# Optimization experiments

Measured on AMD Instinct MI355X. Metric: run time of the kernel, lower is better.

The kernel has to match this reference:

```python
import jax, jax.numpy as jnp
import numpy as np

N_NODES, N_EDGES = 100000, 800000
F_NODE, F_EDGE, N_CLASSES = 128, 16, 10


def _lin(key, fan_in, fan_out, bias=True):
    k1, k2 = jax.random.split(key)
    W = jax.random.normal(k1, (fan_in, fan_out), jnp.float32) * 0.05
    if bias:
        b = jax.random.normal(k2, (fan_out,), jnp.float32) * 0.05
        return W, b
    return (W,)


def setup_inputs() -> dict:
    key = jax.random.key(0)
    ks = jax.random.split(key, 24)
    inp = {
        "x": jax.random.normal(ks[0], (N_NODES, F_NODE), jnp.float32),
        "edge_index": jax.random.randint(ks[1], (2, N_EDGES), 0, N_NODES, jnp.int64 if jax.config.jax_enable_x64 else jnp.int32),
        "edge_attr": jax.random.normal(ks[2], (N_EDGES, F_EDGE), jnp.float32),
    }
    dims = [(F_NODE, 128), (128, 128), (128, 256)]  # (in_channels, out_channels) per layer
    i = 3
    for li, (din, dout) in enumerate(dims, start=1):
        inp[f"Wq{li}"], inp[f"bq{li}"] = _lin(ks[i], din, dout); i += 1
        inp[f"Wk{li}"], inp[f"bk{li}"] = _lin(ks[i], din, dout); i += 1
        inp[f"Wv{li}"], inp[f"bv{li}"] = _lin(ks[i], din, dout); i += 1
        (inp[f"We{li}"],) = _lin(ks[i], F_EDGE, dout, bias=False); i += 1  # PyG lin_edge: bias=False
        inp[f"Ws{li}"], inp[f"bs{li}"] = _lin(ks[i], din, dout); i += 1  # root/skip weight
    inp["Wc"], inp["bc"] = _lin(ks[i], 256, N_CLASSES)
    return inp


def transformer_conv(x, src, dst, edge_attr, Wq, bq, Wk, bk, Wv, bv, We, Ws, bs):
    """PyG TransformerConv, heads=1, concat=True, root_weight=True."""
    N = x.shape[0]
    C = Wq.shape[1]
    q = x @ Wq + bq                      # [N, C]
    k = x @ Wk + bk                      # [N, C]
    v = x @ Wv + bv                      # [N, C]
    e = edge_attr @ We                   # [E, C] edge-conditioned term
    # per-edge attention logits: <q_i, k_j + e_ij> / sqrt(C)
    alpha = jnp.sum(q[dst] * (k[src] + e), axis=-1) / jnp.sqrt(jnp.float32(C))  # [E]
    # segment softmax over edges sharing a destination node
    m = jax.ops.segment_max(alpha, dst, num_segments=N)
    p = jnp.exp(alpha - m[dst])
    s = jax.ops.segment_sum(p, dst, num_segments=N)
    a = p / (s[dst] + 1e-16)
    # scatter-aggregate weighted messages (value_j + edge term)
    out = jax.ops.segment_sum(a[:, None] * (v[src] + e), dst, num_segments=N)  # [N, C]
    return out + x @ Ws + bs             # root/skip connection


def reference(x, edge_index, edge_attr,
              Wq1, bq1, Wk1, bk1, Wv1, bv1, We1, Ws1, bs1,
              Wq2, bq2, Wk2, bk2, Wv2, bv2, We2, Ws2, bs2,
              Wq3, bq3, Wk3, bk3, Wv3, bv3, We3, Ws3, bs3,
              Wc, bc):
    src, dst = edge_index[0], edge_index[1]
    h = transformer_conv(x, src, dst, edge_attr, Wq1, bq1, Wk1, bk1, Wv1, bv1, We1, Ws1, bs1)
    h = jax.nn.relu(h)  # dropout is identity in eval mode
    h = transformer_conv(h, src, dst, edge_attr, Wq2, bq2, Wk2, bk2, Wv2, bv2, We2, Ws2, bs2)
    h = jax.nn.relu(h)
    h = transformer_conv(h, src, dst, edge_attr, Wq3, bq3, Wk3, bk3, Wv3, bv3, We3, Ws3, bs3)
    return h @ Wc + bc                   # [N, num_classes]
```

## Files before the change

kernel.cpp:

```cpp
#include <hip/hip_runtime.h>
#include <math.h>


typedef unsigned int uint;
typedef unsigned short ushort;
typedef __bf16 bf16x8 __attribute__((ext_vector_type(8)));
typedef float f32x4 __attribute__((ext_vector_type(4)));

__device__ __forceinline__ ushort f2bf(float f) {
    uint u = __float_as_uint(f);
    u += 0x7fffu + ((u >> 16) & 1u);
    return (ushort)(u >> 16);
}
__device__ __forceinline__ float bf2f(ushort h) {
    return __uint_as_float(((uint)h) << 16);
}
__device__ __forceinline__ void unpack8(uint4 t, float* o) {
    o[0] = bf2f((ushort)(t.x & 0xffffu)); o[1] = bf2f((ushort)(t.x >> 16));
    o[2] = bf2f((ushort)(t.y & 0xffffu)); o[3] = bf2f((ushort)(t.y >> 16));
    o[4] = bf2f((ushort)(t.z & 0xffffu)); o[5] = bf2f((ushort)(t.z >> 16));
    o[6] = bf2f((ushort)(t.w & 0xffffu)); o[7] = bf2f((ushort)(t.w >> 16));
}

__global__ void k_zero(uint* p, int n) {
    int i = blockIdx.x * 256 + threadIdx.x;
    if (i < n) p[i] = 0u;
}

__global__ void k_hist(const int* __restrict__ dst, uint* __restrict__ counts, int E, int N) {
    int e = blockIdx.x * 256 + threadIdx.x;
    if (e < E) {
        int d = dst[e];
        d = (d < 0) ? 0 : (d >= N ? N - 1 : d);
        atomicAdd(&counts[d], 1u);
    }
}

__global__ void k_scan1(const uint* __restrict__ counts, uint* __restrict__ bsum, int n) {
    __shared__ uint sm[256];
    int tid = threadIdx.x;
    int base = blockIdx.x * 1024 + tid * 4;
    uint s = 0;
#pragma unroll
    for (int j = 0; j < 4; ++j)
        if (base + j < n) s += counts[base + j];
    sm[tid] = s;
    __syncthreads();
    for (int d = 128; d > 0; d >>= 1) {
        if (tid < d) sm[tid] += sm[tid + d];
        __syncthreads();
    }
    if (tid == 0) bsum[blockIdx.x] = sm[0];
}

__global__ void k_scan2(uint* bsum, int nb) {
    if (threadIdx.x == 0 && blockIdx.x == 0) {
        uint run = 0;
        for (int i = 0; i < nb; ++i) { uint v = bsum[i]; bsum[i] = run; run += v; }
    }
}

__global__ void k_scan3(const uint* __restrict__ counts, const uint* __restrict__ bsum,
                        uint* __restrict__ row_ptr, int n, int E) {
    __shared__ uint sm[256];
    int tid = threadIdx.x;
    int base = blockIdx.x * 1024 + tid * 4;
    uint local[4];
    uint s = 0;
#pragma unroll
    for (int j = 0; j < 4; ++j) {
        local[j] = (base + j < n) ? counts[base + j] : 0u;
        s += local[j];
    }
    sm[tid] = s;
    __syncthreads();
    for (int d = 1; d < 256; d <<= 1) {
        uint v = (tid >= d) ? sm[tid - d] : 0u;
        __syncthreads();
        sm[tid] += v;
        __syncthreads();
    }
    uint run = sm[tid] - s + bsum[blockIdx.x];
#pragma unroll
    for (int j = 0; j < 4; ++j)
        if (base + j < n) { row_ptr[base + j] = run; run += local[j]; }
    if (blockIdx.x == 0 && tid == 0) row_ptr[n] = (uint)E;
}

__global__ void k_fill(const int* __restrict__ ei, const uint* __restrict__ row_ptr,
                       uint* __restrict__ cursor, int2* __restrict__ srcid, int E, int N) {
    int e = blockIdx.x * 256 + threadIdx.x;
    if (e >= E) return;
    int s = ei[e];
    int d = ei[E + e];
    s = (s < 0) ? 0 : (s >= N ? N - 1 : s);
    d = (d < 0) ? 0 : (d >= N ? N - 1 : d);
    uint idx = row_ptr[d] + atomicAdd(&cursor[d], 1u);
    srcid[idx] = make_int2(s, e);
}

__global__ void k_cvt(const float4* __restrict__ in, ushort4* __restrict__ outp, int n4) {
    int i = blockIdx.x * 256 + threadIdx.x;
    if (i >= n4) return;
    float4 v = in[i];
    ushort4 o;
    o.x = f2bf(v.x); o.y = f2bf(v.y); o.z = f2bf(v.z); o.w = f2bf(v.w);
    outp[i] = o;
}

__global__ void k_packg(const float* __restrict__ Wq, const float* __restrict__ bq,
                        const float* __restrict__ We, float* __restrict__ Wgf,
                        float* __restrict__ bgf, int C) {
    int id = blockIdx.x * 256 + threadIdx.x;
    if (id < 2048) {
        int k = id >> 4, f = id & 15;
        float s = 0.f;
        for (int c = 0; c < C; ++c) s = fmaf(Wq[k * C + c], We[f * C + c], s);
        Wgf[id] = s;
    } else if (id < 2064) {
        int f = id - 2048;
        float s = 0.f;
        for (int c = 0; c < C; ++c) s = fmaf(bq[c], We[f * C + c], s);
        bgf[f] = s;
    }
}

__global__ void k_packw(const float* __restrict__ Wq, const float* __restrict__ Wk,
                        const float* __restrict__ Wv, const float* __restrict__ Ws,
                        const float* __restrict__ Wgf, ushort* __restrict__ Bp, int C) {
    int nct = (4 * C + 16) >> 4;
    int total = 4 * nct * 512;
    int id = blockIdx.x * 256 + threadIdx.x;
    if (id >= total) return;
    int j = id & 7;
    int rest = id >> 3;
    int lane = rest & 63;
    rest >>= 6;
    int ct = rest % nct;
    int kt = rest / nct;
    int k = kt * 32 + ((lane >> 4) << 3) + j;
    int c = (ct << 4) + (lane & 15);
    float w;
    if (c < 4 * C) {
        int mat = c / C, cc = c % C;
        const float* W = (mat == 0) ? Wq : (mat == 1) ? Wk : (mat == 2) ? Wv : Ws;
        w = W[k * C + cc];
    } else {
        w = Wgf[k * 16 + (c - 4 * C)];
    }
    Bp[id] = f2bf(w);
}

__global__ void k_bias(const float* __restrict__ bq, const float* __restrict__ bk,
                       const float* __restrict__ bv, const float* __restrict__ bs,
                       const float* __restrict__ bgf, float* __restrict__ outp, int C) {
    int c = blockIdx.x * 256 + threadIdx.x;
    if (c >= 4 * C + 16) return;
    float v;
    if (c < 4 * C) {
        int mat = c / C, cc = c % C;
        const float* b = (mat == 0) ? bq : (mat == 1) ? bk : (mat == 2) ? bv : bs;
        v = b[cc];
    } else {
        v = bgf[c - 4 * C];
    }
    outp[c] = v;
}

__global__ __launch_bounds__(256) void k_gemm(const ushort* __restrict__ A,
                                              const ushort* __restrict__ Bp,
                                              const float* __restrict__ bias,
                                              ushort* __restrict__ H,
                                              ushort* __restrict__ S,
                                              ushort* __restrict__ g, int C) {
    int fourC = 4 * C, threeC = 3 * C;
    int P = fourC + 16;
    int nct = P >> 4;
    int lane = threadIdx.x & 63;
    int wave = threadIdx.x >> 6;
    int quad = lane >> 4;
    int r = lane & 15;
    int m0 = blockIdx.y << 4;
    int c0 = (blockIdx.x << 8) + (wave << 6);
    int ct0 = c0 >> 4;
    if (ct0 >= nct) return;
    int row = m0 + r;

    f32x4 acc[4];
#pragma unroll
    for (int i = 0; i < 4; ++i) acc[i] = (f32x4){0.f, 0.f, 0.f, 0.f};

#pragma unroll
    for (int kk = 0; kk < 4; ++kk) {
        bf16x8 a = *(const bf16x8*)(A + (size_t)row * 128 + kk * 32 + (quad << 3));
#pragma unroll
        for (int i = 0; i < 4; ++i) {
            if (ct0 + i < nct) {
                bf16x8 b = *(const bf16x8*)(Bp + ((size_t)((kk * nct + ct0 + i) << 6) + lane) * 8);
                acc[i] = __builtin_amdgcn_mfma_f32_16x16x32_bf16(a, b, acc[i], 0, 0, 0);
            }
        }
    }
#pragma unroll
    for (int i = 0; i < 4; ++i) {
        int cc = c0 + (i << 4) + r;
        if (cc >= P) continue;
        float bi = bias[cc];
#pragma unroll
        for (int reg = 0; reg < 4; ++reg) {
            int rr = m0 + (quad << 2) + reg;
            ushort val = f2bf(acc[i][reg] + bi);
            if (cc < threeC)      H[(size_t)rr * threeC + cc] = val;
            else if (cc < fourC)  S[(size_t)rr * C + (cc - threeC)] = val;
            else                  g[(size_t)rr * 16 + (cc - fourC)] = val;
        }
    }
}

template <int C, int GSIZE, bool RELU>
__global__ __launch_bounds__(256, 6) void k_edge(const ushort* __restrict__ H,
                                                 ushort* __restrict__ S,
                                                 const ushort* __restrict__ g,
                                                 const uint* __restrict__ row_ptr,
                                                 const int2* __restrict__ srcid,
                                                 const float* __restrict__ eattr,
                                                 const float* __restrict__ We,
                                                 int N) {
    constexpr int VR = C / GSIZE;
    constexpr int TH = 3 * C;
    constexpr int GPB = 256 / GSIZE;
    __shared__ float swex[GPB][17];
    const float scale = (C == 128) ? 0.08838834764831843f : 0.0625f;
    const float foldk = 16.0f / (float)GSIZE;

    int lane = threadIdx.x & (GSIZE - 1);
    int grp = threadIdx.x / GSIZE;
    int f = lane & 15;
    int node = blockIdx.x * GPB + grp;
    if (node >= N) return;

    float q[VR];
    {
        uint4 tt = *(const uint4*)(H + (size_t)node * TH + lane * VR);
        unpack8(tt, q);
    }
    float gl = bf2f(g[(size_t)node * 16 + f]);
    uint beg = row_ptr[node], end = row_ptr[node + 1];

    float l = 0.f, w = 0.f;
    float acc[VR];
#pragma unroll
    for (int j = 0; j < VR; ++j) acc[j] = 0.f;

    for (uint t = beg; t < end; t += 2) {
        bool has1 = (t + 1 < end);
        int2 se0 = srcid[t];
        int2 se1 = has1 ? srcid[t + 1] : se0;
        float at0 = eattr[(size_t)se0.y * 16 + f];
        float at1 = eattr[(size_t)se1.y * 16 + f];
        uint4 k0 = *(const uint4*)(H + (size_t)se0.x * TH + C + lane * VR);
        uint4 v0 = *(const uint4*)(H + (size_t)se0.x * TH + 2 * C + lane * VR);
        uint4 k1, v1;
        if (has1) {
            k1 = *(const uint4*)(H + (size_t)se1.x * TH + C + lane * VR);
            v1 = *(const uint4*)(H + (size_t)se1.x * TH + 2 * C + lane * VR);
        }
        float kf[VR];
        unpack8(k0, kf);
        float p0 = foldk * at0 * gl;
#pragma unroll
        for (int j = 0; j < VR; ++j) p0 = fmaf(q[j], kf[j], p0);
        float p1 = 0.f;
        if (has1) {
            unpack8(k1, kf);
            p1 = foldk * at1 * gl;
#pragma unroll
            for (int j = 0; j < VR; ++j) p1 = fmaf(q[j], kf[j], p1);
        }
        p0 += __shfl_xor(p0, 1); p1 += __shfl_xor(p1, 1);
        p0 += __shfl_xor(p0, 2); p1 += __shfl_xor(p1, 2);
        p0 += __shfl_xor(p0, 4); p1 += __shfl_xor(p1, 4);
        p0 += __shfl_xor(p0, 8); p1 += __shfl_xor(p1, 8);
        if (GSIZE == 32) { p0 += __shfl_xor(p0, 16); p1 += __shfl_xor(p1, 16); }
        float e0 = __expf(p0 * scale);
        float e1 = has1 ? __expf(p1 * scale) : 0.f;
        l += e0 + e1;
        w = fmaf(e0, at0, w);
        w = fmaf(e1, at1, w);
        float vf[VR];
        unpack8(v0, vf);
#pragma unroll
        for (int j = 0; j < VR; ++j) acc[j] = fmaf(e0, vf[j], acc[j]);
        if (has1) {
            unpack8(v1, vf);
#pragma unroll
            for (int j = 0; j < VR; ++j) acc[j] = fmaf(e1, vf[j], acc[j]);
        }
    }

    float inv = 1.f / (l + 1e-16f);
    if (lane < 16) swex[grp][lane] = w;
    float ew[VR];
#pragma unroll
    for (int j = 0; j < VR; ++j) ew[j] = 0.f;
#pragma unroll
    for (int f2 = 0; f2 < 16; ++f2) {
        float wf = swex[grp][f2];
        const float* wrow = We + f2 * C + lane * VR;
#pragma unroll
        for (int u = 0; u < VR / 4; ++u) {
            float4 cv = *(const float4*)(wrow + u * 4);
            ew[u * 4 + 0] = fmaf(wf, cv.x, ew[u * 4 + 0]);
            ew[u * 4 + 1] = fmaf(wf, cv.y, ew[u * 4 + 1]);
            ew[u * 4 + 2] = fmaf(wf, cv.z, ew[u * 4 + 2]);
            ew[u * 4 + 3] = fmaf(wf, cv.w, ew[u * 4 + 3]);
        }
    }
    ushort* srow = S + (size_t)node * C + lane * VR;
    uint4 skv = *(const uint4*)srow;
    float sk[8];
    unpack8(skv, sk);
    uint4 ov;
    uint* op = (uint*)&ov;
#pragma unroll
    for (int h = 0; h < 4; ++h) {
        float o0 = (acc[2 * h] + ew[2 * h]) * inv + sk[2 * h];
        float o1 = (acc[2 * h + 1] + ew[2 * h + 1]) * inv + sk[2 * h + 1];
        if (RELU) { o0 = fmaxf(o0, 0.f); o1 = fmaxf(o1, 0.f); }
        op[h] = (uint)f2bf(o0) | ((uint)f2bf(o1) << 16);
    }
    *(uint4*)srow = ov;
}

__global__ void k_cls(const ushort* __restrict__ h, const float* __restrict__ Wc,
                      const float* __restrict__ bc, float* __restrict__ outp, int N) {
    int t = blockIdx.x * 256 + threadIdx.x;
    int node = t >> 4;
    int c = t & 15;
    if (node >= N || c >= 10) return;
    const ushort* hr = h + (size_t)node * 256;
    float acc = 0.f;
#pragma unroll 4
    for (int k4 = 0; k4 < 64; ++k4) {
        uint2 u = *(const uint2*)(hr + k4 * 4);
        float h0 = bf2f((ushort)(u.x & 0xffffu));
        float h1 = bf2f((ushort)(u.x >> 16));
        float h2 = bf2f((ushort)(u.y & 0xffffu));
        float h3 = bf2f((ushort)(u.y >> 16));
        int kb = k4 * 4;
        acc = fmaf(h0, Wc[(kb + 0) * 10 + c], acc);
        acc = fmaf(h1, Wc[(kb + 1) * 10 + c], acc);
        acc = fmaf(h2, Wc[(kb + 2) * 10 + c], acc);
        acc = fmaf(h3, Wc[(kb + 3) * 10 + c], acc);
    }
    outp[node * 10 + c] = acc + bc[c];
}

extern "C" void kernel_launch(void* const* d_in, const int* in_sizes, int n_in,
                              void* d_out, int out_size, void* d_ws, size_t ws_size,
                              hipStream_t stream) {
    const float* x = (const float*)d_in[0];
    const int* ei = (const int*)d_in[1];
    const float* eattr = (const float*)d_in[2];
    const int N = in_sizes[0] / 128;
    const int E = in_sizes[1] / 2;

    const float* Wq[3], *bq[3], *Wk[3], *bk[3], *Wv[3], *bv[3], *We[3], *Ws[3], *bs[3];
    for (int li = 0; li < 3; ++li) {
        int base = 3 + li * 9;
        Wq[li] = (const float*)d_in[base + 0];
        bq[li] = (const float*)d_in[base + 1];
        Wk[li] = (const float*)d_in[base + 2];
        bk[li] = (const float*)d_in[base + 3];
        Wv[li] = (const float*)d_in[base + 4];
        bv[li] = (const float*)d_in[base + 5];
        We[li] = (const float*)d_in[base + 6];
        Ws[li] = (const float*)d_in[base + 7];
        bs[li] = (const float*)d_in[base + 8];
    }
    const float* Wc = (const float*)d_in[30];
    const float* bc = (const float*)d_in[31];

    size_t off = 0;
    char* base = (char*)d_ws;
    auto alloc = [&](size_t bytes) -> void* {
        void* p = base + off;
        off = (off + bytes + 255) & ~(size_t)255;
        return p;
    };
    ushort* SA = (ushort*)alloc((size_t)N * 256 * 2);
    ushort* SB = (ushort*)alloc((size_t)N * 128 * 2);
    ushort* H  = (ushort*)alloc((size_t)N * 768 * 2);
    ushort* gbuf = (ushort*)alloc((size_t)N * 16 * 2);
    ushort* Bp = (ushort*)alloc(140000 * 2);
    float* biasc = (float*)alloc(1040 * 4);
    float* Wgf = (float*)alloc(2048 * 4);
    float* bgf = (float*)alloc(16 * 4);
    uint* row_ptr = (uint*)alloc((size_t)(N + 1) * 4);
    uint* counts = (uint*)alloc((size_t)N * 4);
    uint* cursor = (uint*)alloc((size_t)N * 4);
    uint* bsum = (uint*)alloc(1024 * 4);
    int2* srcid = (int2*)alloc((size_t)E * 8);

    ushort* xb = SB;

    int nb = (N + 1023) / 1024;

    k_zero<<<(N + 255) / 256, 256, 0, stream>>>(counts, N);
    k_zero<<<(N + 255) / 256, 256, 0, stream>>>(cursor, N);
    k_hist<<<(E + 255) / 256, 256, 0, stream>>>(ei + E, counts, E, N);
    k_scan1<<<nb, 256, 0, stream>>>(counts, bsum, N);
    k_scan2<<<1, 64, 0, stream>>>(bsum, nb);
    k_scan3<<<nb, 256, 0, stream>>>(counts, bsum, row_ptr, N, E);
    k_fill<<<(E + 255) / 256, 256, 0, stream>>>(ei, row_ptr, cursor, srcid, E, N);

    int n4 = N * 128 / 4;
    k_cvt<<<(n4 + 255) / 256, 256, 0, stream>>>((const float4*)x, (ushort4*)xb, n4);

    for (int li = 0; li < 3; ++li) {
        int C = (li == 2) ? 256 : 128;
        int P = 4 * C + 16;
        int packTotal = 4 * (P >> 4) * 512;
        const ushort* A = (li == 0) ? xb : (li == 1) ? SA : SB;
        ushort* Sout = (li == 1) ? SB : SA;

        k_packg<<<9, 256, 0, stream>>>(Wq[li], bq[li], We[li], Wgf, bgf, C);
        k_packw<<<(packTotal + 255) / 256, 256, 0, stream>>>(Wq[li], Wk[li], Wv[li], Ws[li], Wgf, Bp, C);
        k_bias<<<(P + 255) / 256, 256, 0, stream>>>(bq[li], bk[li], bv[li], bs[li], bgf, biasc, C);
        k_gemm<<<dim3((P + 255) / 256, N / 16), 256, 0, stream>>>(A, Bp, biasc, H, Sout, gbuf, C);
        if (li == 2)
            k_edge<256, 32, false><<<(N * 32 + 255) / 256, 256, 0, stream>>>(H, Sout, gbuf, row_ptr, srcid, eattr, We[li], N);
        else
            k_edge<128, 16, true><<<(N * 16 + 255) / 256, 256, 0, stream>>>(H, Sout, gbuf, row_ptr, srcid, eattr, We[li], N);
    }

    k_cls<<<(N * 16 + 255) / 256, 256, 0, stream>>>(SA, Wc, bc, (float*)d_out, N);
}
```

Baseline: 1.030 ms.

## Switch intermediates from bf16 to fp16 and unroll edge loop by four

Stores projected node features in fp16 instead of bf16, uses the fp16 MFMA for the fused projection GEMM, and computes attention dot products with packed fdot2 instructions. The edge aggregation loop now handles four edges per iteration with clamped indices, which raises memory-level parallelism for the gathered K/V rows. Value accumulation and the edge-term expansion use packed two-wide float FMAs. Activations that exceed the fp16 range could overflow, and the wider unroll raises register pressure.

```diff
diff --git a/kernel.cpp b/kernel.cpp
--- a/kernel.cpp
+++ b/kernel.cpp
@@ -4,23 +4,31 @@
 
 typedef unsigned int uint;
 typedef unsigned short ushort;
-typedef __bf16 bf16x8 __attribute__((ext_vector_type(8)));
+typedef _Float16 f16x8 __attribute__((ext_vector_type(8)));
+typedef _Float16 h16x2 __attribute__((ext_vector_type(2)));
 typedef float f32x4 __attribute__((ext_vector_type(4)));
-
-__device__ __forceinline__ ushort f2bf(float f) {
-    uint u = __float_as_uint(f);
-    u += 0x7fffu + ((u >> 16) & 1u);
-    return (ushort)(u >> 16);
-}
-__device__ __forceinline__ float bf2f(ushort h) {
-    return __uint_as_float(((uint)h) << 16);
-}
-__device__ __forceinline__ void unpack8(uint4 t, float* o) {
-    o[0] = bf2f((ushort)(t.x & 0xffffu)); o[1] = bf2f((ushort)(t.x >> 16));
-    o[2] = bf2f((ushort)(t.y & 0xffffu)); o[3] = bf2f((ushort)(t.y >> 16));
-    o[4] = bf2f((ushort)(t.z & 0xffffu)); o[5] = bf2f((ushort)(t.z >> 16));
-    o[6] = bf2f((ushort)(t.w & 0xffffu)); o[7] = bf2f((ushort)(t.w >> 16));
-}
+typedef float f32x2 __attribute__((ext_vector_type(2)));
+
+__device__ __forceinline__ ushort f2h(float f) {
+    return __builtin_bit_cast(ushort, (_Float16)f);
+}
+__device__ __forceinline__ float h2f(ushort h) {
+    return (float)__builtin_bit_cast(_Float16, h);
+}
+__device__ __forceinline__ h16x2 bch2(uint u) { return __builtin_bit_cast(h16x2, u); }
+__device__ __forceinline__ f32x2 cvt2(uint u) {
+    h16x2 h = bch2(u);
+    return (f32x2){(float)h.x, (float)h.y};
+}
+
+#if __has_builtin(__builtin_amdgcn_fdot2)
+#define FDOT2(a, b, c) __builtin_amdgcn_fdot2((a), (b), (c), false)
+#else
+__device__ __forceinline__ float fdot2_sw(h16x2 a, h16x2 b, float c) {
+    return fmaf((float)a.x, (float)b.x, fmaf((float)a.y, (float)b.y, c));
+}
+#define FDOT2(a, b, c) fdot2_sw((a), (b), (c))
+#endif
 
 __global__ void k_zero(uint* p, int n) {
     int i = blockIdx.x * 256 + threadIdx.x;
@@ -104,7 +112,7 @@
     if (i >= n4) return;
     float4 v = in[i];
     ushort4 o;
-    o.x = f2bf(v.x); o.y = f2bf(v.y); o.z = f2bf(v.z); o.w = f2bf(v.w);
+    o.x = f2h(v.x); o.y = f2h(v.y); o.z = f2h(v.z); o.w = f2h(v.w);
     outp[i] = o;
 }
 
@@ -148,7 +156,7 @@
     } else {
         w = Wgf[k * 16 + (c - 4 * C)];
     }
-    Bp[id] = f2bf(w);
+    Bp[id] = f2h(w);
 }
 
 __global__ void k_bias(const float* __restrict__ bq, const float* __restrict__ bk,
@@ -192,12 +200,12 @@
 
 #pragma unroll
     for (int kk = 0; kk < 4; ++kk) {
-        bf16x8 a = *(const bf16x8*)(A + (size_t)row * 128 + kk * 32 + (quad << 3));
+        f16x8 a = *(const f16x8*)(A + (size_t)row * 128 + kk * 32 + (quad << 3));
 #pragma unroll
         for (int i = 0; i < 4; ++i) {
             if (ct0 + i < nct) {
-                bf16x8 b = *(const bf16x8*)(Bp + ((size_t)((kk * nct + ct0 + i) << 6) + lane) * 8);
-                acc[i] = __builtin_amdgcn_mfma_f32_16x16x32_bf16(a, b, acc[i], 0, 0, 0);
+                f16x8 b = *(const f16x8*)(Bp + ((size_t)((kk * nct + ct0 + i) << 6) + lane) * 8);
+                acc[i] = __builtin_amdgcn_mfma_f32_16x16x32_f16(a, b, acc[i], 0, 0, 0);
             }
         }
     }
@@ -209,7 +217,7 @@
 #pragma unroll
         for (int reg = 0; reg < 4; ++reg) {
             int rr = m0 + (quad << 2) + reg;
-            ushort val = f2bf(acc[i][reg] + bi);
+            ushort val = f2h(acc[i][reg] + bi);
             if (cc < threeC)      H[(size_t)rr * threeC + cc] = val;
             else if (cc < fourC)  S[(size_t)rr * C + (cc - threeC)] = val;
             else                  g[(size_t)rr * 16 + (cc - fourC)] = val;
@@ -238,96 +246,117 @@
     int f = lane & 15;
     int node = blockIdx.x * GPB + grp;
     if (node >= N) return;
-
-    float q[VR];
-    {
-        uint4 tt = *(const uint4*)(H + (size_t)node * TH + lane * VR);
-        unpack8(tt, q);
-    }
-    float gl = bf2f(g[(size_t)node * 16 + f]);
+    int lvr = lane * VR;
+
+    uint4 qv = *(const uint4*)(H + (size_t)node * TH + lvr);
+    h16x2 q0 = bch2(qv.x), q1 = bch2(qv.y), q2 = bch2(qv.z), q3 = bch2(qv.w);
+    float gl = h2f(g[(size_t)node * 16 + f]);
+    float fg = foldk * gl;
     uint beg = row_ptr[node], end = row_ptr[node + 1];
 
     float l = 0.f, w = 0.f;
-    float acc[VR];
-#pragma unroll
-    for (int j = 0; j < VR; ++j) acc[j] = 0.f;
-
-    for (uint t = beg; t < end; t += 2) {
-        bool has1 = (t + 1 < end);
-        int2 se0 = srcid[t];
-        int2 se1 = has1 ? srcid[t + 1] : se0;
-        float at0 = eattr[(size_t)se0.y * 16 + f];
-        float at1 = eattr[(size_t)se1.y * 16 + f];
-        uint4 k0 = *(const uint4*)(H + (size_t)se0.x * TH + C + lane * VR);
-        uint4 v0 = *(const uint4*)(H + (size_t)se0.x * TH + 2 * C + lane * VR);
-        uint4 k1, v1;
-        if (has1) {
-            k1 = *(const uint4*)(H + (size_t)se1.x * TH + C + lane * VR);
-            v1 = *(const uint4*)(H + (size_t)se1.x * TH + 2 * C + lane * VR);
+    f32x2 acc[4];
+#pragma unroll
+    for (int j = 0; j < 4; ++j) acc[j] = (f32x2){0.f, 0.f};
+
+    for (uint t = beg; t < end; t += 4) {
+        uint t1 = (t + 1 < end) ? t + 1 : t;
+        uint t2 = (t + 2 < end) ? t + 2 : t;
+        uint t3 = (t + 3 < end) ? t + 3 : t;
+        int2 s0 = srcid[t], s1 = srcid[t1], s2 = srcid[t2], s3 = srcid[t3];
+        float at0 = eattr[(size_t)s0.y * 16 + f];
+        float at1 = eattr[(size_t)s1.y * 16 + f];
+        float at2 = eattr[(size_t)s2.y * 16 + f];
+        float at3 = eattr[(size_t)s3.y * 16 + f];
+        const ushort* hb0 = H + (size_t)s0.x * TH + C + lvr;
+        const ushort* hb1 = H + (size_t)s1.x * TH + C + lvr;
+        const ushort* hb2 = H + (size_t)s2.x * TH + C + lvr;
+        const ushort* hb3 = H + (size_t)s3.x * TH + C + lvr;
+        uint4 k0 = *(const uint4*)hb0, v0 = *(const uint4*)(hb0 + C);
+        uint4 k1 = *(const uint4*)hb1, v1 = *(const uint4*)(hb1 + C);
+        uint4 k2 = *(const uint4*)hb2, v2 = *(const uint4*)(hb2 + C);
+        uint4 k3 = *(const uint4*)hb3, v3 = *(const uint4*)(hb3 + C);
+
+        float p0 = at0 * fg, p1 = at1 * fg, p2 = at2 * fg, p3 = at3 * fg;
+        p0 = FDOT2(q0, bch2(k0.x), p0); p0 = FDOT2(q1, bch2(k0.y), p0);
+        p0 = FDOT2(q2, bch2(k0.z), p0); p0 = FDOT2(q3, bch2(k0.w), p0);
+        p1 = FDOT2(q0, bch2(k1.x), p1); p1 = FDOT2(q1, bch2(k1.y), p1);
+        p1 = FDOT2(q2, bch2(k1.z), p1); p1 = FDOT2(q3, bch2(k1.w), p1);
+        p2 = FDOT2(q0, bch2(k2.x), p2); p2 = FDOT2(q1, bch2(k2.y), p2);
+        p2 = FDOT2(q2, bch2(k2.z), p2); p2 = FDOT2(q3, bch2(k2.w), p2);
+        p3 = FDOT2(q0, bch2(k3.x), p3); p3 = FDOT2(q1, bch2(k3.y), p3);
+        p3 = FDOT2(q2, bch2(k3.z), p3); p3 = FDOT2(q3, bch2(k3.w), p3);
+
+        p0 += __shfl_xor(p0, 1); p1 += __shfl_xor(p1, 1);
+        p2 += __shfl_xor(p2, 1); p3 += __shfl_xor(p3, 1);
+        p0 += __shfl_xor(p0, 2); p1 += __shfl_xor(p1, 2);
+        p2 += __shfl_xor(p2, 2); p3 += __shfl_xor(p3, 2);
+        p0 += __shfl_xor(p0, 4); p1 += __shfl_xor(p1, 4);
+        p2 += __shfl_xor(p2, 4); p3 += __shfl_xor(p3, 4);
+        p0 += __shfl_xor(p0, 8); p1 += __shfl_xor(p1, 8);
+        p2 += __shfl_xor(p2, 8); p3 += __shfl_xor(p3, 8);
+        if (GSIZE == 32) {
+            p0 += __shfl_xor(p0, 16); p1 += __shfl_xor(p1, 16);
+            p2 += __shfl_xor(p2, 16); p3 += __shfl_xor(p3, 16);
         }
-        float kf[VR];
-        unpack8(k0, kf);
-        float p0 = foldk * at0 * gl;
-#pragma unroll
-        for (int j = 0; j < VR; ++j) p0 = fmaf(q[j], kf[j], p0);
-        float p1 = 0.f;
-        if (has1) {
-            unpack8(k1, kf);
-            p1 = foldk * at1 * gl;
-#pragma unroll
-            for (int j = 0; j < VR; ++j) p1 = fmaf(q[j], kf[j], p1);
-        }
-        p0 += __shfl_xor(p0, 1); p1 += __shfl_xor(p1, 1);
-        p0 += __shfl_xor(p0, 2); p1 += __shfl_xor(p1, 2);
-        p0 += __shfl_xor(p0, 4); p1 += __shfl_xor(p1, 4);
-        p0 += __shfl_xor(p0, 8); p1 += __shfl_xor(p1, 8);
-        if (GSIZE == 32) { p0 += __shfl_xor(p0, 16); p1 += __shfl_xor(p1, 16); }
         float e0 = __expf(p0 * scale);
-        float e1 = has1 ? __expf(p1 * scale) : 0.f;
-        l += e0 + e1;
-        w = fmaf(e0, at0, w);
-        w = fmaf(e1, at1, w);
-        float vf[VR];
-        unpack8(v0, vf);
-#pragma unroll
-        for (int j = 0; j < VR; ++j) acc[j] = fmaf(e0, vf[j], acc[j]);
-        if (has1) {
-            unpack8(v1, vf);
-#pragma unroll
-            for (int j = 0; j < VR; ++j) acc[j] = fmaf(e1, vf[j], acc[j]);
-        }
+        float e1 = (t + 1 < end) ? __expf(p1 * scale) : 0.f;
+        float e2 = (t + 2 < end) ? __expf(p2 * scale) : 0.f;
+        float e3 = (t + 3 < end) ? __expf(p3 * scale) : 0.f;
+        l += (e0 + e1) + (e2 + e3);
+        w = fmaf(e0, at0, w); w = fmaf(e1, at1, w);
+        w = fmaf(e2, at2, w); w = fmaf(e3, at3, w);
+        f32x2 eb;
+        eb = (f32x2){e0, e0};
+        acc[0] = __builtin_elementwise_fma(cvt2(v0.x), eb, acc[0]);
+        acc[1] = __builtin_elementwise_fma(cvt2(v0.y), eb, acc[1]);
+        acc[2] = __builtin_elementwise_fma(cvt2(v0.z), eb, acc[2]);
+        acc[3] = __builtin_elementwise_fma(cvt2(v0.w), eb, acc[3]);
+        eb = (f32x2){e1, e1};
+        acc[0] = __builtin_elementwise_fma(cvt2(v1.x), eb, acc[0]);
+        acc[1] = __builtin_elementwise_fma(cvt2(v1.y), eb, acc[1]);
+        acc[2] = __builtin_elementwise_fma(cvt2(v1.z), eb, acc[2]);
+        acc[3] = __builtin_elementwise_fma(cvt2(v1.w), eb, acc[3]);
+        eb = (f32x2){e2, e2};
+        acc[0] = __builtin_elementwise_fma(cvt2(v2.x), eb, acc[0]);
+        acc[1] = __builtin_elementwise_fma(cvt2(v2.y), eb, acc[1]);
+        acc[2] = __builtin_elementwise_fma(cvt2(v2.z), eb, acc[2]);
+        acc[3] = __builtin_elementwise_fma(cvt2(v2.w), eb, acc[3]);
+        eb = (f32x2){e3, e3};
+        acc[0] = __builtin_elementwise_fma(cvt2(v3.x), eb, acc[0]);
+        acc[1] = __builtin_elementwise_fma(cvt2(v3.y), eb, acc[1]);
+        acc[2] = __builtin_elementwise_fma(cvt2(v3.z), eb, acc[2]);
+        acc[3] = __builtin_elementwise_fma(cvt2(v3.w), eb, acc[3]);
     }
 
     float inv = 1.f / (l + 1e-16f);
     if (lane < 16) swex[grp][lane] = w;
-    float ew[VR];
-#pragma unroll
-    for (int j = 0; j < VR; ++j) ew[j] = 0.f;
-#pragma unroll
-    for (int f2 = 0; f2 < 16; ++f2) {
-        float wf = swex[grp][f2];
-        const float* wrow = We + f2 * C + lane * VR;
-#pragma unroll
-        for (int u = 0; u < VR / 4; ++u) {
-            float4 cv = *(const float4*)(wrow + u * 4);
-            ew[u * 4 + 0] = fmaf(wf, cv.x, ew[u * 4 + 0]);
-            ew[u * 4 + 1] = fmaf(wf, cv.y, ew[u * 4 + 1]);
-            ew[u * 4 + 2] = fmaf(wf, cv.z, ew[u * 4 + 2]);
-            ew[u * 4 + 3] = fmaf(wf, cv.w, ew[u * 4 + 3]);
-        }
-    }
-    ushort* srow = S + (size_t)node * C + lane * VR;
+    f32x2 ew[4];
+#pragma unroll
+    for (int j = 0; j < 4; ++j) ew[j] = (f32x2){0.f, 0.f};
+#pragma unroll
+    for (int f2i = 0; f2i < 16; ++f2i) {
+        float wfs = swex[grp][f2i];
+        f32x2 wf = (f32x2){wfs, wfs};
+        const f32x4* wrow = (const f32x4*)(We + f2i * C + lvr);
+        f32x4 c0 = wrow[0], c1 = wrow[1];
+        ew[0] = __builtin_elementwise_fma(c0.lo, wf, ew[0]);
+        ew[1] = __builtin_elementwise_fma(c0.hi, wf, ew[1]);
+        ew[2] = __builtin_elementwise_fma(c1.lo, wf, ew[2]);
+        ew[3] = __builtin_elementwise_fma(c1.hi, wf, ew[3]);
+    }
+    ushort* srow = S + (size_t)node * C + lvr;
     uint4 skv = *(const uint4*)srow;
-    float sk[8];
-    unpack8(skv, sk);
+    const uint* sp = (const uint*)&skv;
     uint4 ov;
     uint* op = (uint*)&ov;
 #pragma unroll
-    for (int h = 0; h < 4; ++h) {
-        float o0 = (acc[2 * h] + ew[2 * h]) * inv + sk[2 * h];
-        float o1 = (acc[2 * h + 1] + ew[2 * h + 1]) * inv + sk[2 * h + 1];
+    for (int hh = 0; hh < 4; ++hh) {
+        f32x2 sk = cvt2(sp[hh]);
+        float o0 = (acc[hh].x + ew[hh].x) * inv + sk.x;
+        float o1 = (acc[hh].y + ew[hh].y) * inv + sk.y;
         if (RELU) { o0 = fmaxf(o0, 0.f); o1 = fmaxf(o1, 0.f); }
-        op[h] = (uint)f2bf(o0) | ((uint)f2bf(o1) << 16);
+        op[hh] = (uint)f2h(o0) | ((uint)f2h(o1) << 16);
     }
     *(uint4*)srow = ov;
 }
@@ -343,15 +372,13 @@
 #pragma unroll 4
     for (int k4 = 0; k4 < 64; ++k4) {
         uint2 u = *(const uint2*)(hr + k4 * 4);
-        float h0 = bf2f((ushort)(u.x & 0xffffu));
-        float h1 = bf2f((ushort)(u.x >> 16));
-        float h2 = bf2f((ushort)(u.y & 0xffffu));
-        float h3 = bf2f((ushort)(u.y >> 16));
+        f32x2 a01 = cvt2(u.x);
+        f32x2 a23 = cvt2(u.y);
         int kb = k4 * 4;
-        acc = fmaf(h0, Wc[(kb + 0) * 10 + c], acc);
-        acc = fmaf(h1, Wc[(kb + 1) * 10 + c], acc);
-        acc = fmaf(h2, Wc[(kb + 2) * 10 + c], acc);
-        acc = fmaf(h3, Wc[(kb + 3) * 10 + c], acc);
+        acc = fmaf(a01.x, Wc[(kb + 0) * 10 + c], acc);
+        acc = fmaf(a01.y, Wc[(kb + 1) * 10 + c], acc);
+        acc = fmaf(a23.x, Wc[(kb + 2) * 10 + c], acc);
+        acc = fmaf(a23.y, Wc[(kb + 3) * 10 + c], acc);
     }
     outp[node * 10 + c] = acc + bc[c];
 }
```

New measurement: 1.027 ms. About the same (-0.3%).
